# Kernel optimization log

Measured on AMD Instinct MI355X. Metric: run time of the kernel, lower is better.

Reference implementation:

```python
import jax, jax.numpy as jnp
import numpy as np
import math
from jax import lax

B, C, BINS, W = 2, 8, 1024, 512
HEADS = 8
HD = BINS // HEADS            # 128 head dim
ROT = HD // 2                 # rotary rot_dim = bins//num_heads//2 = 64


def setup_inputs() -> dict:
    key = jax.random.key(0)
    k1, k2, k3, k4, k5 = jax.random.split(key, 5)
    s_lin = 1.0 / math.sqrt(BINS)
    return {
        "x": jax.random.normal(k1, (B, C, BINS, W), dtype=jnp.float32),
        "Wq_lin": jax.random.uniform(k2, (C, BINS, BINS), jnp.float32, -s_lin, s_lin),
        "Wq_conv": jax.random.normal(k3, (C, C, 1, 3), dtype=jnp.float32) * 0.1,
        "bq_conv": jax.random.normal(k4, (C,), dtype=jnp.float32) * 0.1,
        "Wout": jax.random.uniform(k5, (C, BINS, BINS), jnp.float32, -s_lin, s_lin),
    }


def _mc_linear(x, Wc):
    # separable MultichannelLinear: out[b,c,o,w] = sum_i W[c,o,i] x[b,c,i,w]
    return jnp.einsum('coi,bciw->bcow', Wc, x)


def _proj(x, Wl, Wc, bc):
    y = _mc_linear(x, Wl)
    y = lax.conv_general_dilated(y, Wc, (1, 1), ((0, 0), (1, 1)),
                                 dimension_numbers=('NCHW', 'OIHW', 'NCHW'))
    return y + bc[None, :, None, None]


def _to_heads(y):
    # [b,c,bins,w] -> [b,c,H,w,hd]
    b, c, _, w = y.shape
    return y.transpose(0, 1, 3, 2).reshape(b, c, w, HEADS, HD).transpose(0, 1, 3, 2, 4)


def _rotary(t):
    # lucidrains RotaryEmbedding(dim=ROT, freqs_for='lang'): rotate first ROT dims over seq axis (-2)
    inv = 1.0 / (10000.0 ** (jnp.arange(0, ROT, 2, dtype=jnp.float32) / ROT))  # [ROT//2]
    pos = jnp.arange(t.shape[-2], dtype=jnp.float32)
    f = jnp.repeat(pos[:, None] * inv[None, :], 2, axis=-1)  # [w, ROT] interleaved repeat
    cos, sin = jnp.cos(f), jnp.sin(f)
    left, right = t[..., :ROT], t[..., ROT:]
    x1, x2 = left[..., 0::2], left[..., 1::2]
    rot = jnp.stack([-x2, x1], axis=-1).reshape(left.shape)
    return jnp.concatenate([left * cos + rot * sin, right], axis=-1)


def reference(x, Wq_lin, Wq_conv, bq_conv, Wout):
    b, c, h, w = x.shape
    # NOTE: original forward uses q_proj for q, k AND v (k_proj/v_proj unused)
    qp = _proj(x, Wq_lin, Wq_conv, bq_conv)
    qh = _to_heads(qp)                       # [b,c,H,w,hd]
    q = _rotary(qh)
    k = _rotary(qh)
    v = qh
    scale = 1.0 / math.sqrt(h)               # custom scale: sqrt(bins), not sqrt(head_dim)
    qk = jnp.einsum('bchqd,bchkd->bchqk', q, k) * scale
    a = jnp.einsum('bchqk,bchkd->bchqd', jax.nn.softmax(qk, axis=-1), v)
    # [b,c,H,w,hd] -> [b,c,bins,w]
    a = a.transpose(0, 1, 3, 2, 4).reshape(b, c, w, h).transpose(0, 1, 3, 2)
    return _mc_linear(a, Wout)
```

## Files before the change

kernel.cpp:

```cpp
#include <hip/hip_runtime.h>
#include <cstddef>

#define Bb 2
#define Cc_ 8
#define BINS 1024
#define Ww 512
#define HEADS 8
#define HD 128
#define NELEM (Bb*Cc_*BINS*Ww)
#define SLOT ((size_t)NELEM + 640)

typedef __attribute__((ext_vector_type(8)))  __bf16 bf16x8;
typedef __attribute__((ext_vector_type(4)))  __bf16 bf16x4;
typedef __attribute__((ext_vector_type(4)))  float  f32x4;
typedef __attribute__((ext_vector_type(16))) float  f32x16;
#define MFMA32(a,b,c) __builtin_amdgcn_mfma_f32_32x32x16_bf16(a,b,c,0,0,0)

__device__ __forceinline__ void async16(const __bf16* g, __bf16* l) {
    __builtin_amdgcn_global_load_lds(
        (const __attribute__((address_space(1))) void*)g,
        (__attribute__((address_space(3))) void*)l, 16, 0, 0);
}

__global__ void __launch_bounds__(256) wcast(const float* __restrict__ Wq,
                                             const float* __restrict__ Wout,
                                             __bf16* __restrict__ Wqb,
                                             __bf16* __restrict__ Woutb) {
    int bid = blockIdx.x;
    const float* in = (bid < 4096) ? Wq : Wout;
    __bf16* outp    = (bid < 4096) ? Wqb : Woutb;
    size_t i = ((size_t)(bid & 4095) * 256 + threadIdx.x) * 8;
    f32x4 a = __builtin_nontemporal_load((const f32x4*)&in[i]);
    f32x4 b = __builtin_nontemporal_load((const f32x4*)&in[i + 4]);
    bf16x8 o = {(__bf16)a[0], (__bf16)a[1], (__bf16)a[2], (__bf16)a[3],
                (__bf16)b[0], (__bf16)b[1], (__bf16)b[2], (__bf16)b[3]};
    *(bf16x8*)&outp[i] = o;
}

__global__ void __launch_bounds__(256) xpose(const float* __restrict__ x,
                                             __bf16* __restrict__ xT) {
    int b2 = blockIdx.x;
    int t = threadIdx.x;
    int w0 = (b2 & 7) * 64;
    int i0 = ((b2 >> 3) & 15) * 64;
    int bc = b2 >> 7;
    const float* src = x + (size_t)bc * BINS * Ww;
    __bf16* dst = xT + (size_t)bc * Ww * BINS;
    __shared__ float T[64][65];
    #pragma unroll
    for (int pass = 0; pass < 4; pass++) {
        int idx = t + pass * 256;
        int il = idx >> 4, ch = idx & 15;
        f32x4 v = __builtin_nontemporal_load(
            (const f32x4*)&src[(size_t)(i0 + il) * Ww + w0 + ch * 4]);
        T[il][ch * 4 + 0] = v[0]; T[il][ch * 4 + 1] = v[1];
        T[il][ch * 4 + 2] = v[2]; T[il][ch * 4 + 3] = v[3];
    }
    __syncthreads();
    #pragma unroll
    for (int pass = 0; pass < 2; pass++) {
        int idx = t + pass * 256;
        int wl = idx >> 3, ch = idx & 7;
        bf16x8 o;
        #pragma unroll
        for (int j = 0; j < 8; j++) o[j] = (__bf16)T[ch * 8 + j][wl];
        *(bf16x8*)&dst[(size_t)(w0 + wl) * BINS + i0 + ch * 8] = o;
    }
}

template<bool BF16OUT>
__global__ void __launch_bounds__(256) gemm32(const __bf16* __restrict__ Wall,
                                              const __bf16* __restrict__ Bt,
                                              void* __restrict__ Yv) {
    int bc = blockIdx.z, c = bc & 7;
    const __bf16* A  = Wall + (size_t)c  * BINS * BINS;
    const __bf16* Bm = Bt   + (size_t)bc * Ww * BINS;
    int n0 = blockIdx.x * 128, m0 = blockIdx.y * 128;

    __shared__ __align__(16) char smem[32768];
    __bf16* Asm = (__bf16*)smem;
    __bf16* Bsm = (__bf16*)(smem + 16384);

    int t = threadIdx.x, w = t >> 6, l = t & 63;
    int l31 = l & 31, h = l >> 5;
    int wm = w >> 1, wn = w & 1;

    int rowS[4], colS[4];
    #pragma unroll
    for (int j = 0; j < 4; j++) {
        int p = j * 256 + w * 64 + l;
        int r = p >> 3, cs = (p & 7) ^ (r & 7);
        rowS[j] = r; colS[j] = cs * 8;
    }

    f32x16 acc[2][2];
    #pragma unroll
    for (int a = 0; a < 2; a++)
        #pragma unroll
        for (int b = 0; b < 2; b++)
            #pragma unroll
            for (int r = 0; r < 16; r++) acc[a][b][r] = 0.f;

    for (int k0 = 0; k0 < BINS; k0 += 64) {
        __syncthreads();
        #pragma unroll
        for (int j = 0; j < 4; j++) {
            async16(A  + (size_t)(m0 + rowS[j]) * BINS + k0 + colS[j],
                    Asm + (j * 256 + w * 64) * 8);
            async16(Bm + (size_t)(n0 + rowS[j]) * BINS + k0 + colS[j],
                    Bsm + (j * 256 + w * 64) * 8);
        }
        __syncthreads();
        bf16x8 af[2][4], bfr[2][4];
        #pragma unroll
        for (int mt = 0; mt < 2; mt++)
            #pragma unroll
            for (int kc = 0; kc < 4; kc++) {
                int row = wm * 64 + mt * 32 + l31;
                int ch = (kc * 2 + h) ^ (row & 7);
                af[mt][kc] = *(bf16x8*)&Asm[row * 64 + ch * 8];
            }
        #pragma unroll
        for (int nt = 0; nt < 2; nt++)
            #pragma unroll
            for (int kc = 0; kc < 4; kc++) {
                int row = wn * 64 + nt * 32 + l31;
                int ch = (kc * 2 + h) ^ (row & 7);
                bfr[nt][kc] = *(bf16x8*)&Bsm[row * 64 + ch * 8];
            }
        #pragma unroll
        for (int kc = 0; kc < 4; kc++)
            #pragma unroll
            for (int mt = 0; mt < 2; mt++)
                #pragma unroll
                for (int nt = 0; nt < 2; nt++)
                    acc[mt][nt] = MFMA32(af[mt][kc], bfr[nt][kc], acc[mt][nt]);
    }

    __syncthreads();
    if constexpr (BF16OUT) {
        __bf16* Ob = (__bf16*)smem;
        __bf16* Cm = (__bf16*)Yv + (size_t)bc * BINS * Ww;
        #pragma unroll
        for (int mt = 0; mt < 2; mt++)
            #pragma unroll
            for (int nt = 0; nt < 2; nt++)
                #pragma unroll
                for (int reg = 0; reg < 16; reg++) {
                    int ml = wm * 64 + mt * 32 + (reg & 3) + 8 * (reg >> 2) + 4 * h;
                    int nl = wn * 64 + nt * 32 + l31;
                    Ob[ml * 128 + nl] = (__bf16)acc[mt][nt][reg];
                }
        __syncthreads();
        #pragma unroll
        for (int pass = 0; pass < 8; pass++) {
            int idx = t + pass * 256;
            int row = idx >> 4, ch = idx & 15;
            *(bf16x8*)&Cm[(size_t)(m0 + row) * Ww + n0 + ch * 8] =
                *(bf16x8*)&Ob[row * 128 + ch * 8];
        }
    } else {
        float* Of = (float*)smem;
        float* Cm = (float*)Yv + (size_t)bc * BINS * Ww;
        #pragma unroll
        for (int half = 0; half < 2; half++) {
            if (wm == half) {
                #pragma unroll
                for (int mt = 0; mt < 2; mt++)
                    #pragma unroll
                    for (int nt = 0; nt < 2; nt++)
                        #pragma unroll
                        for (int reg = 0; reg < 16; reg++) {
                            int ml = mt * 32 + (reg & 3) + 8 * (reg >> 2) + 4 * h;
                            int nl = wn * 64 + nt * 32 + l31;
                            Of[ml * 128 + nl] = acc[mt][nt][reg];
                        }
            }
            __syncthreads();
            #pragma unroll
            for (int pass = 0; pass < 8; pass++) {
                int idx = t + pass * 256;
                int row = idx >> 5, c4 = idx & 31;
                __builtin_nontemporal_store(
                    *(const f32x4*)&Of[row * 128 + c4 * 4],
                    (f32x4*)&Cm[(size_t)(m0 + half * 64 + row) * Ww + n0 + c4 * 4]);
            }
            __syncthreads();
        }
    }
}

__global__ void __launch_bounds__(256) conv1x3_reg(const __bf16* __restrict__ y,
                                                   const float* __restrict__ Wc,
                                                   const float* __restrict__ bias,
                                                   __bf16* __restrict__ vt) {
    int tid = blockIdx.x * 256 + threadIdx.x;
    int wc = tid & 63;
    int h  = (tid >> 6) & 1023;
    int b  = tid >> 16;
    int w0 = wc * 8;

    float ym[8][8], yl[8], yr[8];
    #pragma unroll
    for (int ci = 0; ci < 8; ci++) {
        const __bf16* row = y + ((size_t)(b * 8 + ci) * BINS + h) * Ww;
        bf16x8 v = *(const bf16x8*)&row[w0];
        #pragma unroll
        for (int j = 0; j < 8; j++) ym[ci][j] = (float)v[j];
        yl[ci] = (w0 > 0)   ? (float)row[w0 - 1] : 0.f;
        yr[ci] = (w0 < 504) ? (float)row[w0 + 8] : 0.f;
    }
    #pragma unroll
    for (int co = 0; co < 8; co++) {
        float acc[8];
        float bv = bias[co];
        #pragma unroll
        for (int j = 0; j < 8; j++) acc[j] = bv;
        #pragma unroll
        for (int ci = 0; ci < 8; ci++) {
            float wa = Wc[(co * 8 + ci) * 3 + 0];
            float wb = Wc[(co * 8 + ci) * 3 + 1];
            float wcc = Wc[(co * 8 + ci) * 3 + 2];
            acc[0] += yl[ci] * wa;
            #pragma unroll
            for (int j = 1; j < 8; j++) acc[j] += ym[ci][j - 1] * wa;
            #pragma unroll
            for (int j = 0; j < 8; j++) acc[j] += ym[ci][j] * wb;
            #pragma unroll
            for (int j = 0; j < 7; j++) acc[j] += ym[ci][j + 1] * wcc;
            acc[7] += yr[ci] * wcc;
        }
        bf16x8 o;
        #pragma unroll
        for (int j = 0; j < 8; j++) o[j] = (__bf16)acc[j];
        *(bf16x8*)&vt[((size_t)(b * 8 + co) * BINS + h) * Ww + w0] = o;
    }
}

__global__ void __launch_bounds__(256) rotary_transpose(const __bf16* __restrict__ vt,
                                                        __bf16* __restrict__ qrot) {
    int p0  = blockIdx.x * 64;
    int bch = blockIdx.y;
    int t = threadIdx.x;
    __shared__ float T[64 * 129];

    const __bf16* src = vt + (size_t)bch * HD * Ww;
    for (int pass = 0; pass < 4; pass++) {
        int idx = t + pass * 256;
        int d = idx >> 3, ch = idx & 7;
        bf16x8 v = *(const bf16x8*)&src[(size_t)d * Ww + p0 + ch * 8];
        #pragma unroll
        for (int j = 0; j < 8; j++) T[(ch * 8 + j) * 129 + d] = (float)v[j];
    }
    __syncthreads();
    for (int pass = 0; pass < 4; pass++) {
        int idx = t + pass * 256;
        int p = idx >> 4, chunk = idx & 15;
        float pos = (float)(p0 + p);
        bf16x8 o;
        if (chunk < 8) {
            #pragma unroll
            for (int j = 0; j < 8; j += 2) {
                int d = chunk * 8 + j;
                int jj = d >> 1;
                float inv = __expf(-(2.0f * jj / 64.0f) * 9.210340371976184f);
                float sn, cs;
                __sincosf(pos * inv, &sn, &cs);
                float x1 = T[p * 129 + d];
                float x2 = T[p * 129 + d + 1];
                o[j]     = (__bf16)(x1 * cs - x2 * sn);
                o[j + 1] = (__bf16)(x2 * cs + x1 * sn);
            }
        } else {
            #pragma unroll
            for (int j = 0; j < 8; j++)
                o[j] = (__bf16)T[p * 129 + chunk * 8 + j];
        }
        *(bf16x8*)&qrot[((size_t)bch * Ww + p0 + p) * HD + chunk * 8] = o;
    }
}

__global__ void __launch_bounds__(256, 2) attn32(const __bf16* __restrict__ qrot,
                                                 const __bf16* __restrict__ vt,
                                                 __bf16* __restrict__ attnT) {
    int bid = blockIdx.x;
    int bch = bid & 127, q0 = (bid >> 7) * 128;
    int t = threadIdx.x, wv = t >> 6, lane = t & 63;
    int l31 = lane & 31, h = lane >> 5;

    __shared__ __align__(16) char smem[49152];
    __bf16* Ks  = (__bf16*)smem;
    __bf16* Vts = (__bf16*)(smem + 16384);
    __bf16* Psw = (__bf16*)(smem + 32768) + wv * 2048;

    const __bf16* qb = qrot + (size_t)bch * Ww * HD;
    const __bf16* vb = vt   + (size_t)bch * HD * Ww;

    int qrow = q0 + wv * 32 + l31;
    bf16x8 qf[8];
    #pragma unroll
    for (int c = 0; c < 8; c++) {
        bf16x8 v = *(const bf16x8*)&qb[(size_t)qrow * HD + c * 16 + h * 8];
        #pragma unroll
        for (int j = 0; j < 8; j++) v[j] = (__bf16)((float)v[j] * 0.03125f);
        qf[c] = v;
    }

    f32x16 oacc[4];
    #pragma unroll
    for (int dt = 0; dt < 4; dt++)
        #pragma unroll
        for (int r = 0; r < 16; r++) oacc[dt][r] = 0.f;
    float m_st = -1e30f, l_st = 0.f;

    for (int kt = 0; kt < 8; kt++) {
        int k0 = kt * 64;
        __syncthreads();
        #pragma unroll
        for (int i = 0; i < 4; i++) {
            int p = wv * 256 + i * 64 + lane;
            int r  = p >> 4, cs  = ((p & 15) ^ (r & 15)) * 8;
            async16(qb + (size_t)(k0 + r) * HD + cs, Ks + (wv * 256 + i * 64) * 8);
            int r2 = p >> 3, cs2 = ((p & 7) ^ (r2 & 7)) * 8;
            async16(vb + (size_t)r2 * Ww + k0 + cs2, Vts + (wv * 256 + i * 64) * 8);
        }
        __syncthreads();

        f32x16 st[2];
        #pragma unroll
        for (int t2 = 0; t2 < 2; t2++)
            #pragma unroll
            for (int r = 0; r < 16; r++) st[t2][r] = 0.f;
        #pragma unroll
        for (int c = 0; c < 8; c++)
            #pragma unroll
            for (int t2 = 0; t2 < 2; t2++) {
                int row = t2 * 32 + l31;
                int ch = (c * 2 + h) ^ (row & 15);
                bf16x8 ak = *(bf16x8*)&Ks[row * 128 + ch * 8];
                st[t2] = MFMA32(ak, qf[c], st[t2]);
            }

        float mx = -1e30f;
        #pragma unroll
        for (int t2 = 0; t2 < 2; t2++)
            #pragma unroll
            for (int r = 0; r < 16; r++) mx = fmaxf(mx, st[t2][r]);
        mx = fmaxf(mx, __shfl_xor(mx, 32));
        float mnew = fmaxf(m_st, mx);
        float alpha = __expf(m_st - mnew);
        float sum = 0.f;
        #pragma unroll
        for (int t2 = 0; t2 < 2; t2++)
            #pragma unroll
            for (int r = 0; r < 16; r++) {
                float p = __expf(st[t2][r] - mnew);
                st[t2][r] = p;
                sum += p;
            }
        sum += __shfl_xor(sum, 32);
        l_st = l_st * alpha + sum;
        m_st = mnew;

        #pragma unroll
        for (int t2 = 0; t2 < 2; t2++)
            #pragma unroll
            for (int g = 0; g < 4; g++) {
                bf16x4 pk = {(__bf16)st[t2][4 * g],     (__bf16)st[t2][4 * g + 1],
                             (__bf16)st[t2][4 * g + 2], (__bf16)st[t2][4 * g + 3]};
                int ch = (t2 * 4 + g) ^ (l31 & 7);
                *(bf16x4*)&Psw[l31 * 64 + ch * 8 + 4 * h] = pk;
            }
        #pragma unroll
        for (int dt = 0; dt < 4; dt++)
            #pragma unroll
            for (int r = 0; r < 16; r++) oacc[dt][r] *= alpha;

        #pragma unroll
        for (int kc = 0; kc < 4; kc++) {
            int chp = (kc * 2 + h) ^ (l31 & 7);
            bf16x8 bp = *(bf16x8*)&Psw[l31 * 64 + chp * 8];
            #pragma unroll
            for (int dt = 0; dt < 4; dt++) {
                int row = dt * 32 + l31;
                int cv = (kc * 2 + h) ^ (row & 7);
                bf16x8 av = *(bf16x8*)&Vts[row * 64 + cv * 8];
                oacc[dt] = MFMA32(av, bp, oacc[dt]);
            }
        }
    }

    __syncthreads();
    __bf16* Ob = (__bf16*)smem + wv * 4096;
    float linv = 1.f / l_st;
    #pragma unroll
    for (int dt = 0; dt < 4; dt++)
        #pragma unroll
        for (int g = 0; g < 4; g++) {
            bf16x4 pk = {(__bf16)(oacc[dt][4 * g] * linv),
                         (__bf16)(oacc[dt][4 * g + 1] * linv),
                         (__bf16)(oacc[dt][4 * g + 2] * linv),
                         (__bf16)(oacc[dt][4 * g + 3] * linv)};
            int ch = (dt * 4 + g) ^ (l31 & 15);
            *(bf16x4*)&Ob[l31 * 128 + ch * 8 + 4 * h] = pk;
        }
    int bc = bch >> 3, h0 = bch & 7;
    #pragma unroll
    for (int i = 0; i < 8; i++) {
        int p = i * 64 + lane;
        int rr = p >> 4, cc = p & 15;
        int cs = cc ^ (rr & 15);
        bf16x8 v = *(bf16x8*)&Ob[rr * 128 + cs * 8];
        *(bf16x8*)&attnT[((size_t)bc * Ww + q0 + wv * 32 + rr) * BINS + h0 * HD + cc * 8] = v;
    }
}

extern "C" void kernel_launch(void* const* d_in, const int* in_sizes, int n_in,
                              void* d_out, int out_size, void* d_ws, size_t ws_size,
                              hipStream_t stream) {
    const float* x       = (const float*)d_in[0];
    const float* Wq_lin  = (const float*)d_in[1];
    const float* Wq_conv = (const float*)d_in[2];
    const float* bq_conv = (const float*)d_in[3];
    const float* Wout    = (const float*)d_in[4];
    float* out = (float*)d_out;

    __bf16* U = (__bf16*)d_ws;
    __bf16* Wq_bf   = U + 0 * SLOT;
    __bf16* xT      = U + 1 * SLOT;
    __bf16* Wout_bf = U + 2 * SLOT;
    __bf16* y       = U + 3 * SLOT;
    __bf16* vtb     = U + 4 * SLOT;
    __bf16* qrot    = U + 5 * SLOT;
    __bf16* attnT   = U + 3 * SLOT;

    wcast<<<dim3(8192), 256, 0, stream>>>(Wq_lin, Wout, Wq_bf, Wout_bf);
    xpose<<<dim3(2048), 256, 0, stream>>>(x, xT);
    gemm32<true><<<dim3(Ww / 128, BINS / 128, Bb * Cc_), 256, 0, stream>>>(Wq_bf, xT, y);
    conv1x3_reg<<<dim3(Bb * BINS * 64 / 256), 256, 0, stream>>>(y, Wq_conv, bq_conv, vtb);
    rotary_transpose<<<dim3(Ww / 64, Bb * Cc_ * HEADS), 256, 0, stream>>>(vtb, qrot);
    attn32<<<dim3((Ww / 128) * 128), 256, 0, stream>>>(qrot, vtb, attnT);
    gemm32<false><<<dim3(Ww / 128, BINS / 128, Bb * Cc_), 256, 0, stream>>>(Wout_bf, attnT, out);
}
```

Before: 235.1 us.

## Use 512-thread GEMM blocks with remapped block order for L2 locality

```diff
diff --git a/kernel.cpp b/kernel.cpp
--- a/kernel.cpp
+++ b/kernel.cpp
@@ -69,49 +69,56 @@
 }
 
 template<bool BF16OUT>
-__global__ void __launch_bounds__(256) gemm32(const __bf16* __restrict__ Wall,
-                                              const __bf16* __restrict__ Bt,
-                                              void* __restrict__ Yv) {
-    int bc = blockIdx.z, c = bc & 7;
+__global__ void __launch_bounds__(512, 4) gemm32(const __bf16* __restrict__ Wall,
+                                                 const __bf16* __restrict__ Bt,
+                                                 void* __restrict__ Yv) {
+    int lin = blockIdx.x;
+    int k8  = lin & 7;
+    int q   = lin >> 3;
+    int j8  = q & 7;
+    int phi = q >> 3;
+    int p   = phi * 8 + k8;
+    int c   = p & 7, m0 = (p >> 3) * 128;
+    int n0  = (j8 & 3) * 128;
+    int bc  = (j8 >> 2) * 8 + c;
+
     const __bf16* A  = Wall + (size_t)c  * BINS * BINS;
     const __bf16* Bm = Bt   + (size_t)bc * Ww * BINS;
-    int n0 = blockIdx.x * 128, m0 = blockIdx.y * 128;
 
     __shared__ __align__(16) char smem[32768];
     __bf16* Asm = (__bf16*)smem;
     __bf16* Bsm = (__bf16*)(smem + 16384);
 
     int t = threadIdx.x, w = t >> 6, l = t & 63;
-    int l31 = l & 31, h = l >> 5;
-    int wm = w >> 1, wn = w & 1;
-
-    int rowS[4], colS[4];
-    #pragma unroll
-    for (int j = 0; j < 4; j++) {
-        int p = j * 256 + w * 64 + l;
-        int r = p >> 3, cs = (p & 7) ^ (r & 7);
+    int l31 = l & 31, h = (l >> 5) & 1;
+    int wm = w >> 2, wn = w & 3;
+
+    int rowS[2], colS[2];
+    #pragma unroll
+    for (int j = 0; j < 2; j++) {
+        int p2 = j * 512 + t;
+        int r = p2 >> 3, cs = (p2 & 7) ^ (r & 7);
         rowS[j] = r; colS[j] = cs * 8;
     }
 
-    f32x16 acc[2][2];
-    #pragma unroll
-    for (int a = 0; a < 2; a++)
-        #pragma unroll
-        for (int b = 0; b < 2; b++)
-            #pragma unroll
-            for (int r = 0; r < 16; r++) acc[a][b][r] = 0.f;
+    f32x16 acc[2];
+    #pragma unroll
+    for (int mt = 0; mt < 2; mt++)
+        #pragma unroll
+        for (int r = 0; r < 16; r++) acc[mt][r] = 0.f;
 
     for (int k0 = 0; k0 < BINS; k0 += 64) {
         __syncthreads();
         #pragma unroll
-        for (int j = 0; j < 4; j++) {
+        for (int j = 0; j < 2; j++) {
             async16(A  + (size_t)(m0 + rowS[j]) * BINS + k0 + colS[j],
-                    Asm + (j * 256 + w * 64) * 8);
+                    Asm + (j * 512 + t) * 8);
             async16(Bm + (size_t)(n0 + rowS[j]) * BINS + k0 + colS[j],
-                    Bsm + (j * 256 + w * 64) * 8);
+                    Bsm + (j * 512 + t) * 8);
         }
         __syncthreads();
-        bf16x8 af[2][4], bfr[2][4];
+
+        bf16x8 af[2][4], bfr[4];
         #pragma unroll
         for (int mt = 0; mt < 2; mt++)
             #pragma unroll
@@ -121,20 +128,16 @@
                 af[mt][kc] = *(bf16x8*)&Asm[row * 64 + ch * 8];
             }
         #pragma unroll
-        for (int nt = 0; nt < 2; nt++)
-            #pragma unroll
-            for (int kc = 0; kc < 4; kc++) {
-                int row = wn * 64 + nt * 32 + l31;
-                int ch = (kc * 2 + h) ^ (row & 7);
-                bfr[nt][kc] = *(bf16x8*)&Bsm[row * 64 + ch * 8];
-            }
+        for (int kc = 0; kc < 4; kc++) {
+            int row = wn * 32 + l31;
+            int ch = (kc * 2 + h) ^ (row & 7);
+            bfr[kc] = *(bf16x8*)&Bsm[row * 64 + ch * 8];
+        }
         #pragma unroll
         for (int kc = 0; kc < 4; kc++)
             #pragma unroll
             for (int mt = 0; mt < 2; mt++)
-                #pragma unroll
-                for (int nt = 0; nt < 2; nt++)
-                    acc[mt][nt] = MFMA32(af[mt][kc], bfr[nt][kc], acc[mt][nt]);
+                acc[mt] = MFMA32(af[mt][kc], bfr[kc], acc[mt]);
     }
 
     __syncthreads();
@@ -144,17 +147,15 @@
         #pragma unroll
         for (int mt = 0; mt < 2; mt++)
             #pragma unroll
-            for (int nt = 0; nt < 2; nt++)
-                #pragma unroll
-                for (int reg = 0; reg < 16; reg++) {
-                    int ml = wm * 64 + mt * 32 + (reg & 3) + 8 * (reg >> 2) + 4 * h;
-                    int nl = wn * 64 + nt * 32 + l31;
-                    Ob[ml * 128 + nl] = (__bf16)acc[mt][nt][reg];
-                }
+            for (int reg = 0; reg < 16; reg++) {
+                int ml = wm * 64 + mt * 32 + (reg & 3) + 8 * (reg >> 2) + 4 * h;
+                int nl = wn * 32 + l31;
+                Ob[ml * 128 + nl] = (__bf16)acc[mt][reg];
+            }
         __syncthreads();
         #pragma unroll
-        for (int pass = 0; pass < 8; pass++) {
-            int idx = t + pass * 256;
+        for (int pass = 0; pass < 4; pass++) {
+            int idx = t + pass * 512;
             int row = idx >> 4, ch = idx & 15;
             *(bf16x8*)&Cm[(size_t)(m0 + row) * Ww + n0 + ch * 8] =
                 *(bf16x8*)&Ob[row * 128 + ch * 8];
@@ -168,18 +169,16 @@
                 #pragma unroll
                 for (int mt = 0; mt < 2; mt++)
                     #pragma unroll
-                    for (int nt = 0; nt < 2; nt++)
-                        #pragma unroll
-                        for (int reg = 0; reg < 16; reg++) {
-                            int ml = mt * 32 + (reg & 3) + 8 * (reg >> 2) + 4 * h;
-                            int nl = wn * 64 + nt * 32 + l31;
-                            Of[ml * 128 + nl] = acc[mt][nt][reg];
-                        }
+                    for (int reg = 0; reg < 16; reg++) {
+                        int ml = mt * 32 + (reg & 3) + 8 * (reg >> 2) + 4 * h;
+                        int nl = wn * 32 + l31;
+                        Of[ml * 128 + nl] = acc[mt][reg];
+                    }
             }
             __syncthreads();
             #pragma unroll
-            for (int pass = 0; pass < 8; pass++) {
-                int idx = t + pass * 256;
+            for (int pass = 0; pass < 4; pass++) {
+                int idx = t + pass * 512;
                 int row = idx >> 5, c4 = idx & 31;
                 __builtin_nontemporal_store(
                     *(const f32x4*)&Of[row * 128 + c4 * 4],
@@ -436,9 +435,9 @@
 
     wcast<<<dim3(8192), 256, 0, stream>>>(Wq_lin, Wout, Wq_bf, Wout_bf);
     xpose<<<dim3(2048), 256, 0, stream>>>(x, xT);
-    gemm32<true><<<dim3(Ww / 128, BINS / 128, Bb * Cc_), 256, 0, stream>>>(Wq_bf, xT, y);
+    gemm32<true><<<dim3(512), 512, 0, stream>>>(Wq_bf, xT, y);
     conv1x3_reg<<<dim3(Bb * BINS * 64 / 256), 256, 0, stream>>>(y, Wq_conv, bq_conv, vtb);
     rotary_transpose<<<dim3(Ww / 64, Bb * Cc_ * HEADS), 256, 0, stream>>>(vtb, qrot);
     attn32<<<dim3((Ww / 128) * 128), 256, 0, stream>>>(qrot, vtb, attnT);
-    gemm32<false><<<dim3(Ww / 128, BINS / 128, Bb * Cc_), 256, 0, stream>>>(Wout_bf, attnT, out);
-}
+    gemm32<false><<<dim3(512), 512, 0, stream>>>(Wout_bf, attnT, out);
+}
```

Result: faster. 230.1 us (-2.1%).
